# Kernel tuning notes

Hardware: AMD Instinct MI355X
Metric: run time of the kernel (lower is better)

The kernel has to match this reference:

```python
import jax, jax.numpy as jnp
import numpy as np

N_NODES = 50000
N_EDGES = 400000
D_NODE = 256
D_EDGE = 64
LN_EPS = 1e-6  # flax LayerNorm default


def _layer_norm(x, scale, bias):
    mu = jnp.mean(x, axis=-1, keepdims=True)
    var = jnp.mean(jnp.square(x - mu), axis=-1, keepdims=True)
    return (x - mu) * jax.lax.rsqrt(var + LN_EPS) * scale + bias


def _glorot(key, shape):
    fan_in, fan_out = shape
    std = jnp.sqrt(2.0 / (fan_in + fan_out))
    return std * jax.random.normal(key, shape, dtype=jnp.float32)


def setup_inputs() -> dict:
    key = jax.random.key(0)
    ks = jax.random.split(key, 10)
    inp = {
        "nodes": jax.random.normal(ks[0], (N_NODES, D_NODE), dtype=jnp.float32),
        "edges": jax.random.normal(ks[1], (N_EDGES, D_EDGE), dtype=jnp.float32),
        "senders": jax.random.randint(ks[2], (N_EDGES,), 0, N_NODES, dtype=jnp.int32),
        "receivers": jax.random.randint(ks[3], (N_EDGES,), 0, N_NODES, dtype=jnp.int32),
        # message projection (no bias)
        "W_message": _glorot(ks[4], (D_NODE + D_EDGE, D_NODE)),
        # NodeMLP (ReluMLP_skip) with n_features_list_nodes = [256, 256, 256]
        "mlp_W0": _glorot(ks[5], (D_NODE, D_NODE)), "mlp_b0": jnp.zeros((D_NODE,), jnp.float32),
        "mlp_W1": _glorot(ks[6], (D_NODE, D_NODE)), "mlp_b1": jnp.zeros((D_NODE,), jnp.float32),
        "mlp_W2": _glorot(ks[7], (D_NODE, D_NODE)), "mlp_b2": jnp.zeros((D_NODE,), jnp.float32),
        # LayerNorm params
        "ln_aggr_scale": jnp.ones((D_NODE,), jnp.float32), "ln_aggr_bias": jnp.zeros((D_NODE,), jnp.float32),
        "ln_out_scale": jnp.ones((D_NODE,), jnp.float32), "ln_out_bias": jnp.zeros((D_NODE,), jnp.float32),
    }
    return inp


def _relu_mlp_skip(x, Ws, bs):
    # Dense layers; ReLU on all but the last; residual add whenever widths match.
    n = len(Ws)
    for i, (W, b) in enumerate(zip(Ws, bs)):
        y = x @ W + b
        if i < n - 1:
            y = jax.nn.relu(y)
        x = x + y if y.shape[-1] == x.shape[-1] else y
    return x


def reference(nodes, edges, senders, receivers, W_message,
              mlp_W0, mlp_b0, mlp_W1, mlp_b1, mlp_W2, mlp_b2,
              ln_aggr_scale, ln_aggr_bias, ln_out_scale, ln_out_bias):
    total_nodes = nodes.shape[0]
    sender_features = nodes[senders]                      # [E, d] gather
    msg_in = jnp.concatenate([sender_features, edges], axis=-1)  # [E, d+d_e]
    messages = msg_in @ W_message                          # [E, d]
    agg = jax.ops.segment_sum(messages, receivers, num_segments=total_nodes)  # [N, d]
    h = _layer_norm(jax.nn.relu(agg) + nodes, ln_aggr_scale, ln_aggr_bias)
    nodes_out = _relu_mlp_skip(h, [mlp_W0, mlp_W1, mlp_W2], [mlp_b0, mlp_b1, mlp_b2])
    nodes_new = _layer_norm(nodes + nodes_out, ln_out_scale, ln_out_bias)
    return nodes_new
```

## Files before the change

kernel.cpp:

```cpp
#include <hip/hip_runtime.h>

#define NN 50000
#define NE 400000

typedef unsigned short u16;
typedef unsigned int   u32;
typedef __bf16 bf16x4 __attribute__((ext_vector_type(4)));
typedef __bf16 bf16x8 __attribute__((ext_vector_type(8)));
typedef float  f32x4  __attribute__((ext_vector_type(4)));

union ABFrag { bf16x8 v; bf16x4 h[2]; };
union BFrag  { uint4 u; bf16x8 v; };

__device__ __forceinline__ u16 f2bfu(float f) {
  u32 u = __builtin_bit_cast(u32, f);
  return (u16)((u + 0x7FFFu + ((u >> 16) & 1u)) >> 16);
}
__device__ __forceinline__ float bf2f(u16 u) {
  return __builtin_bit_cast(float, (u32)u << 16);
}

__device__ __forceinline__ void pack_one(const float* __restrict__ W,
                                         u16* __restrict__ P, int idx) {
  int k = idx >> 8, n = idx & 255;
  int t = k >> 5, kp = k & 31;
  int g = (kp & 15) >> 2;
  int j = (kp & 3) | ((kp >> 4) << 2);
  P[(((t << 8) + n) << 5) + (g << 3) + j] = f2bfu(W[idx]);
}

#define NB_CVT  12500
#define NB_PACK 1088
#define NB_HIST 1563

__global__ __launch_bounds__(256) void k_prep(
    const float* __restrict__ nodes, u16* __restrict__ nodes_bf,
    const float* __restrict__ Wm, const float* __restrict__ W0,
    const float* __restrict__ W1, const float* __restrict__ W2,
    u16* __restrict__ Pm, u16* __restrict__ P0,
    u16* __restrict__ P1, u16* __restrict__ P2,
    const int* __restrict__ recv, int* __restrict__ cnt)
{
  int b = blockIdx.x, t = threadIdx.x;
  if (b < NB_CVT) {
    int i = b * 256 + t;
    float4 f = ((const float4*)nodes)[i];
    ushort4 o;
    o.x = f2bfu(f.x); o.y = f2bfu(f.y); o.z = f2bfu(f.z); o.w = f2bfu(f.w);
    ((ushort4*)nodes_bf)[i] = o;
  } else if (b < NB_CVT + NB_PACK) {
    int idx = (b - NB_CVT) * 256 + t;
    const int S0 = 320 * 256, S1 = S0 + 65536, S2 = S1 + 65536;
    if (idx < S0)      pack_one(Wm, Pm, idx);
    else if (idx < S1) pack_one(W0, P0, idx - S0);
    else if (idx < S2) pack_one(W1, P1, idx - S1);
    else               pack_one(W2, P2, idx - S2);
  } else {
    int i = (b - NB_CVT - NB_PACK) * 256 + t;
    if (i < NE) atomicAdd(&cnt[recv[i]], 1);
  }
}

__global__ __launch_bounds__(256) void k_scan1(const int* __restrict__ cnt,
                                               int* __restrict__ loc,
                                               int* __restrict__ bsum) {
  __shared__ int sm[256];
  int t = threadIdx.x, i = blockIdx.x * 256 + t;
  int v = (i < NN) ? cnt[i] : 0;
  sm[t] = v;
  __syncthreads();
  #pragma unroll
  for (int d = 1; d < 256; d <<= 1) {
    int x = sm[t];
    int y = (t >= d) ? sm[t - d] : 0;
    __syncthreads();
    sm[t] = x + y;
    __syncthreads();
  }
  if (i < NN) loc[i] = sm[t] - v;
  if (t == 255) bsum[blockIdx.x] = sm[255];
}

__global__ __launch_bounds__(256) void k_scan2(int* __restrict__ bsum,
                                               int* __restrict__ bpre, int nb) {
  __shared__ int sm[256];
  int t = threadIdx.x;
  int v = (t < nb) ? bsum[t] : 0;
  sm[t] = v;
  __syncthreads();
  #pragma unroll
  for (int d = 1; d < 256; d <<= 1) {
    int x = sm[t];
    int y = (t >= d) ? sm[t - d] : 0;
    __syncthreads();
    sm[t] = x + y;
    __syncthreads();
  }
  if (t < nb) bpre[t] = sm[t] - v;
}

__global__ __launch_bounds__(256) void k_scan3(const int* __restrict__ loc,
                                               const int* __restrict__ bpre,
                                               int* __restrict__ offs,
                                               int* __restrict__ cursor) {
  int i = blockIdx.x * 256 + threadIdx.x;
  if (i < NN) {
    int o = loc[i] + bpre[blockIdx.x];
    offs[i] = o;
    cursor[i] = o;
  }
  if (i == NN - 1) offs[NN] = NE;
}

__global__ __launch_bounds__(256) void k_scatter(
    const int* __restrict__ snd, const int* __restrict__ recv,
    int* __restrict__ cursor, int2* __restrict__ s_pair) {
  int e = blockIdx.x * 256 + threadIdx.x;
  if (e < NE) {
    int p = atomicAdd(&cursor[recv[e]], 1);
    int2 pr; pr.x = snd[e]; pr.y = e;
    s_pair[p] = pr;
  }
}

__global__ __launch_bounds__(256) void k_aggr(
    const u16* __restrict__ nodes_bf, const float* __restrict__ edges,
    const int* __restrict__ offs, const int2* __restrict__ s_pair,
    u16* __restrict__ X)
{
  const int node = blockIdx.x * 4 + (threadIdx.x >> 6);
  const int lane = threadIdx.x & 63;
  const int beg = offs[node], end = offs[node + 1];
  float a0 = 0.f, a1 = 0.f, a2 = 0.f, a3 = 0.f, a4 = 0.f;

  for (int jb = beg; jb < end; jb += 8) {
    int j = jb + (lane & 7);
    if (j >= end) j = end - 1;
    int2 pr = s_pair[j];
    const int rem = end - jb;

#define GATHER(K) \
    int s##K = __shfl(pr.x, K); int e##K = __shfl(pr.y, K); \
    ushort4 n##K = *(const ushort4*)(nodes_bf + (size_t)s##K * 256 + (lane << 2)); \
    float v##K = edges[(size_t)e##K * 64 + lane];

    GATHER(0) GATHER(1) GATHER(2) GATHER(3)
    GATHER(4) GATHER(5) GATHER(6) GATHER(7)
#undef GATHER

#define ACCUM(K) \
    if (rem > K) { \
      a0 += bf2f(n##K.x); a1 += bf2f(n##K.y); \
      a2 += bf2f(n##K.z); a3 += bf2f(n##K.w); \
      a4 += v##K; }

    ACCUM(0) ACCUM(1) ACCUM(2) ACCUM(3)
    ACCUM(4) ACCUM(5) ACCUM(6) ACCUM(7)
#undef ACCUM
  }

  u16* xr = X + (size_t)node * 320;
  ushort4 o;
  o.x = f2bfu(a0); o.y = f2bfu(a1); o.z = f2bfu(a2); o.w = f2bfu(a3);
  *(ushort4*)(xr + (lane << 2)) = o;
  xr[256 + lane] = f2bfu(a4);
}

#define AT_ADDR(r, c) (atb + ((((r) * 640) + ((c) * 2)) ^ (((r) & 7) << 4)))

#define WRBT(c, v) do { int _c = (c); \
  int _i = (((_c >> 10) << 13) + ((_c & 3) << 11) + (((_c & 1023) >> 2) << 3)) ^ ((_c & 3) << 4); \
  *(uint4*)&Bt[_i] = (v); } while (0)

#define MFMA_STEP(t) \
  _Pragma("unroll") \
  for (int kk = 0; kk < 2; ++kk) { \
    ABFrag a; \
    const int kc = (((t) * 2 + kk) << 5) + (g << 2); \
    const int m = wr16 + l16; \
    a.h[0] = *(const bf16x4*)AT_ADDR(m, kc); \
    a.h[1] = *(const bf16x4*)AT_ADDR(m, kc + 16); \
    _Pragma("unroll") \
    for (int q = 0; q < 4; ++q) { \
      BFrag b; \
      b.u = *(const uint4*)&Bt[((kk << 13) + (g << 11) + ((wcn + (q << 4) + l16) << 3)) ^ (g << 4)]; \
      acc[q] = __builtin_amdgcn_mfma_f32_16x16x32_bf16(a.v, b.v, acc[q], 0, 0, 0); \
    } \
  }

#define RUN_LAYER(wp, T) do { \
  const u16* pb = (wp) + ((size_t)tid << 3); \
  uint4 p0 = *(const uint4*)(pb); \
  uint4 p1 = *(const uint4*)(pb + 8192); \
  _Pragma("unroll 1") \
  for (int t = 0; t < (T); ++t) { \
    __syncthreads(); \
    WRBT(tid, p0); WRBT(tid + 1024, p1); \
    __syncthreads(); \
    if (t + 1 < (T)) { \
      const u16* nb = pb + ((size_t)(t + 1) << 14); \
      p0 = *(const uint4*)nb; p1 = *(const uint4*)(nb + 8192); \
    } \
    MFMA_STEP(t) \
  } \
} while (0)

#define LN_STATS() do { \
  _Pragma("unroll") \
  for (int r = 0; r < 4; ++r) { \
    float s  = acc[0][r] + acc[1][r] + acc[2][r] + acc[3][r]; \
    float s2 = acc[0][r]*acc[0][r] + acc[1][r]*acc[1][r] + acc[2][r]*acc[2][r] + acc[3][r]*acc[3][r]; \
    s  += __shfl_xor(s, 1);  s  += __shfl_xor(s, 2);  s  += __shfl_xor(s, 4);  s  += __shfl_xor(s, 8); \
    s2 += __shfl_xor(s2, 1); s2 += __shfl_xor(s2, 2); s2 += __shfl_xor(s2, 4); s2 += __shfl_xor(s2, 8); \
    if (l16 == 0) { int m = wr16 + g4 + r; red[m][wc2] = s; red[m][wc2 + 1] = s2; } \
  } \
  __syncthreads(); \
  if (tid < 64) { \
    float s  = red[tid][0] + red[tid][2] + red[tid][4] + red[tid][6]; \
    float s2 = red[tid][1] + red[tid][3] + red[tid][5] + red[tid][7]; \
    float mu  = s * (1.f / 256.f); \
    float var = s2 * (1.f / 256.f) - mu * mu; \
    murs[tid][0] = mu; murs[tid][1] = rsqrtf(var + 1e-6f); \
  } \
  __syncthreads(); \
} while (0)

__global__ __launch_bounds__(1024)
void k_fused(
    const u16* __restrict__ X, const float* __restrict__ nodes,
    const u16* __restrict__ wm, const u16* __restrict__ w0,
    const u16* __restrict__ w1, const u16* __restrict__ w2,
    const float* __restrict__ b0, const float* __restrict__ b1,
    const float* __restrict__ b2,
    const float* __restrict__ lnAs, const float* __restrict__ lnAb,
    const float* __restrict__ lnOs, const float* __restrict__ lnOb,
    float* __restrict__ out)
{
  __shared__ u16 At[64 * 320];
  __shared__ u16 Bt[16384];
  __shared__ float red[64][8];
  __shared__ float murs[64][2];

  const int tid = threadIdx.x;
  const int lane = tid & 63;
  const int w16 = tid >> 6;
  const int wr16 = (w16 >> 2) << 4;
  const int wcn = (w16 & 3) << 6;
  const int wc2 = (w16 & 3) << 1;
  const int l16 = lane & 15, g = lane >> 4, g4 = g << 2;
  const int r0 = blockIdx.x * 64;

  char* const atb = (char*)At;

  #pragma unroll
  for (int it = 0; it < 3; ++it) {
    int c = tid + it * 1024;
    if (c < 2560) {
      int r = c / 40, seg = c - r * 40;
      int row = r0 + r;
      uint4 v = {0u, 0u, 0u, 0u};
      if (row < NN) v = *(const uint4*)(X + (size_t)row * 320 + seg * 8);
      *(uint4*)(atb + ((r * 640 + seg * 16) ^ ((r & 7) << 4))) = v;
    }
  }

  f32x4 acc[4];
  const f32x4 z = {0.f, 0.f, 0.f, 0.f};
  #pragma unroll
  for (int q = 0; q < 4; ++q) acc[q] = z;

  RUN_LAYER(wm, 5);

  #pragma unroll
  for (int q = 0; q < 4; ++q) {
    int n = wcn + (q << 4) + l16;
    #pragma unroll
    for (int r = 0; r < 4; ++r) {
      int row = r0 + wr16 + g4 + r;
      float nv = (row < NN) ? nodes[(size_t)row * 256 + n] : 0.f;
      acc[q][r] = fmaxf(acc[q][r], 0.f) + nv;
    }
  }
  LN_STATS();
  #pragma unroll
  for (int q = 0; q < 4; ++q) {
    int n = wcn + (q << 4) + l16;
    float scl = lnAs[n], bia = lnAb[n];
    #pragma unroll
    for (int r = 0; r < 4; ++r) {
      int m = wr16 + g4 + r;
      float h = (acc[q][r] - murs[m][0]) * murs[m][1] * scl + bia;
      *(u16*)AT_ADDR(m, n) = f2bfu(h);
      acc[q][r] = 0.f;
    }
  }

  #pragma unroll 1
  for (int l = 0; l < 3; ++l) {
    const u16* wp = (l == 0) ? w0 : (l == 1) ? w1 : w2;
    RUN_LAYER(wp, 4);
    __syncthreads();

    if (l < 2) {
      const float* bp = (l == 0) ? b0 : b1;
      #pragma unroll
      for (int q = 0; q < 4; ++q) {
        int n = wcn + (q << 4) + l16;
        float bn = bp[n];
        #pragma unroll
        for (int r = 0; r < 4; ++r) {
          int m = wr16 + g4 + r;
          u16* p = (u16*)AT_ADDR(m, n);
          float xn = bf2f(*p) + fmaxf(acc[q][r] + bn, 0.f);
          *p = f2bfu(xn);
          acc[q][r] = 0.f;
        }
      }
    } else {
      #pragma unroll
      for (int q = 0; q < 4; ++q) {
        int n = wcn + (q << 4) + l16;
        float bn = b2[n];
        #pragma unroll
        for (int r = 0; r < 4; ++r) {
          int m = wr16 + g4 + r;
          int row = r0 + m;
          float nv = (row < NN) ? nodes[(size_t)row * 256 + n] : 0.f;
          acc[q][r] = nv + bf2f(*(const u16*)AT_ADDR(m, n)) + acc[q][r] + bn;
        }
      }
    }
  }

  LN_STATS();
  #pragma unroll
  for (int q = 0; q < 4; ++q) {
    int n = wcn + (q << 4) + l16;
    float scl = lnOs[n], bia = lnOb[n];
    #pragma unroll
    for (int r = 0; r < 4; ++r) {
      int m = wr16 + g4 + r;
      int row = r0 + m;
      if (row < NN)
        out[(size_t)row * 256 + n] =
            (acc[q][r] - murs[m][0]) * murs[m][1] * scl + bia;
    }
  }
}

extern "C" void kernel_launch(void* const* d_in, const int* in_sizes, int n_in,
                              void* d_out, int out_size, void* d_ws, size_t ws_size,
                              hipStream_t stream)
{
  const float* nodes = (const float*)d_in[0];
  const float* edges = (const float*)d_in[1];
  const int* senders = (const int*)d_in[2];
  const int* receivers = (const int*)d_in[3];
  const float* Wmsg = (const float*)d_in[4];
  const float* W0 = (const float*)d_in[5];
  const float* b0 = (const float*)d_in[6];
  const float* W1 = (const float*)d_in[7];
  const float* b1 = (const float*)d_in[8];
  const float* W2 = (const float*)d_in[9];
  const float* b2 = (const float*)d_in[10];
  const float* lnAs = (const float*)d_in[11];
  const float* lnAb = (const float*)d_in[12];
  const float* lnOs = (const float*)d_in[13];
  const float* lnOb = (const float*)d_in[14];
  float* out = (float*)d_out;
  (void)in_sizes; (void)n_in; (void)out_size; (void)ws_size;

  char* w = (char*)d_ws;
  size_t off = 0;
  auto take = [&](size_t b) { void* p = w + off; off += (b + 511) & ~(size_t)511; return p; };

  u16*   nodes_bf = (u16*)take((size_t)NN * 256 * 2);
  u16*   wmsg_p   = (u16*)take(320 * 256 * 2);
  u16*   w0_p     = (u16*)take(256 * 256 * 2);
  u16*   w1_p     = (u16*)take(256 * 256 * 2);
  u16*   w2_p     = (u16*)take(256 * 256 * 2);
  u16*   X        = (u16*)take((size_t)NN * 320 * 2);
  int*   cnt      = (int*)take((size_t)NN * 4);
  int*   loc      = (int*)take((size_t)NN * 4);
  int*   offs     = (int*)take((size_t)(NN + 1) * 4);
  int*   cursor   = (int*)take((size_t)NN * 4);
  int2*  s_pair   = (int2*)take((size_t)NE * 8);
  int*   bsum     = (int*)take(256 * 4);
  int*   bpre     = (int*)take(256 * 4);

  const int NB = (NN + 255) / 256;

  hipMemsetAsync(cnt, 0, (size_t)NN * 4, stream);
  k_prep<<<NB_CVT + NB_PACK + NB_HIST, 256, 0, stream>>>(
      nodes, nodes_bf, Wmsg, W0, W1, W2, wmsg_p, w0_p, w1_p, w2_p,
      receivers, cnt);

  k_scan1<<<NB, 256, 0, stream>>>(cnt, loc, bsum);
  k_scan2<<<1, 256, 0, stream>>>(bsum, bpre, NB);
  k_scan3<<<NB, 256, 0, stream>>>(loc, bpre, offs, cursor);
  k_scatter<<<(NE + 255) / 256, 256, 0, stream>>>(senders, receivers, cursor, s_pair);

  k_aggr<<<NN / 4, 256, 0, stream>>>(nodes_bf, edges, offs, s_pair, X);

  const int MB = (NN + 63) / 64;
  k_fused<<<MB, 1024, 0, stream>>>(X, nodes, wmsg_p, w0_p, w1_p, w2_p,
                                   b0, b1, b2, lnAs, lnAb, lnOs, lnOb, out);
}
```

Measured before the change: 225.7 us.

## Read MFMA weight fragments from global directly and split aggregation across four waves

```diff
diff --git a/kernel.cpp b/kernel.cpp
--- a/kernel.cpp
+++ b/kernel.cpp
@@ -128,80 +128,52 @@
     const int* __restrict__ offs, const int2* __restrict__ s_pair,
     u16* __restrict__ X)
 {
-  const int node = blockIdx.x * 4 + (threadIdx.x >> 6);
-  const int lane = threadIdx.x & 63;
+  __shared__ float part[4][5][64];
+  const int node = blockIdx.x;
+  const int w = threadIdx.x >> 6, lane = threadIdx.x & 63;
   const int beg = offs[node], end = offs[node + 1];
+
   float a0 = 0.f, a1 = 0.f, a2 = 0.f, a3 = 0.f, a4 = 0.f;
-
-  for (int jb = beg; jb < end; jb += 8) {
-    int j = jb + (lane & 7);
-    if (j >= end) j = end - 1;
+  for (int j = beg + w; j < end; j += 4) {
     int2 pr = s_pair[j];
-    const int rem = end - jb;
-
-#define GATHER(K) \
-    int s##K = __shfl(pr.x, K); int e##K = __shfl(pr.y, K); \
-    ushort4 n##K = *(const ushort4*)(nodes_bf + (size_t)s##K * 256 + (lane << 2)); \
-    float v##K = edges[(size_t)e##K * 64 + lane];
-
-    GATHER(0) GATHER(1) GATHER(2) GATHER(3)
-    GATHER(4) GATHER(5) GATHER(6) GATHER(7)
-#undef GATHER
-
-#define ACCUM(K) \
-    if (rem > K) { \
-      a0 += bf2f(n##K.x); a1 += bf2f(n##K.y); \
-      a2 += bf2f(n##K.z); a3 += bf2f(n##K.w); \
-      a4 += v##K; }
-
-    ACCUM(0) ACCUM(1) ACCUM(2) ACCUM(3)
-    ACCUM(4) ACCUM(5) ACCUM(6) ACCUM(7)
-#undef ACCUM
-  }
-
-  u16* xr = X + (size_t)node * 320;
-  ushort4 o;
-  o.x = f2bfu(a0); o.y = f2bfu(a1); o.z = f2bfu(a2); o.w = f2bfu(a3);
-  *(ushort4*)(xr + (lane << 2)) = o;
-  xr[256 + lane] = f2bfu(a4);
+    ushort4 nv = *(const ushort4*)(nodes_bf + (size_t)pr.x * 256 + (lane << 2));
+    float ev = edges[(size_t)pr.y * 64 + lane];
+    a0 += bf2f(nv.x); a1 += bf2f(nv.y); a2 += bf2f(nv.z); a3 += bf2f(nv.w);
+    a4 += ev;
+  }
+  part[w][0][lane] = a0; part[w][1][lane] = a1; part[w][2][lane] = a2;
+  part[w][3][lane] = a3; part[w][4][lane] = a4;
+  __syncthreads();
+  if (w == 0) {
+    a0 = part[0][0][lane] + part[1][0][lane] + part[2][0][lane] + part[3][0][lane];
+    a1 = part[0][1][lane] + part[1][1][lane] + part[2][1][lane] + part[3][1][lane];
+    a2 = part[0][2][lane] + part[1][2][lane] + part[2][2][lane] + part[3][2][lane];
+    a3 = part[0][3][lane] + part[1][3][lane] + part[2][3][lane] + part[3][3][lane];
+    a4 = part[0][4][lane] + part[1][4][lane] + part[2][4][lane] + part[3][4][lane];
+    u16* xr = X + (size_t)node * 320;
+    ushort4 o;
+    o.x = f2bfu(a0); o.y = f2bfu(a1); o.z = f2bfu(a2); o.w = f2bfu(a3);
+    *(ushort4*)(xr + (lane << 2)) = o;
+    xr[256 + lane] = f2bfu(a4);
+  }
 }
 
 #define AT_ADDR(r, c) (atb + ((((r) * 640) + ((c) * 2)) ^ (((r) & 7) << 4)))
 
-#define WRBT(c, v) do { int _c = (c); \
-  int _i = (((_c >> 10) << 13) + ((_c & 3) << 11) + (((_c & 1023) >> 2) << 3)) ^ ((_c & 3) << 4); \
-  *(uint4*)&Bt[_i] = (v); } while (0)
-
-#define MFMA_STEP(t) \
-  _Pragma("unroll") \
-  for (int kk = 0; kk < 2; ++kk) { \
+#define RUN_LAYER_G(wp, T) do { \
+  _Pragma("unroll 1") \
+  for (int t = 0; t < (T); ++t) { \
     ABFrag a; \
-    const int kc = (((t) * 2 + kk) << 5) + (g << 2); \
+    const int kc = ((t) << 5) + (g << 2); \
     const int m = wr16 + l16; \
     a.h[0] = *(const bf16x4*)AT_ADDR(m, kc); \
     a.h[1] = *(const bf16x4*)AT_ADDR(m, kc + 16); \
     _Pragma("unroll") \
     for (int q = 0; q < 4; ++q) { \
       BFrag b; \
-      b.u = *(const uint4*)&Bt[((kk << 13) + (g << 11) + ((wcn + (q << 4) + l16) << 3)) ^ (g << 4)]; \
+      b.u = *(const uint4*)((wp) + ((size_t)((((t) << 8) + wcn + (q << 4) + l16) << 5)) + (g << 3)); \
       acc[q] = __builtin_amdgcn_mfma_f32_16x16x32_bf16(a.v, b.v, acc[q], 0, 0, 0); \
     } \
-  }
-
-#define RUN_LAYER(wp, T) do { \
-  const u16* pb = (wp) + ((size_t)tid << 3); \
-  uint4 p0 = *(const uint4*)(pb); \
-  uint4 p1 = *(const uint4*)(pb + 8192); \
-  _Pragma("unroll 1") \
-  for (int t = 0; t < (T); ++t) { \
-    __syncthreads(); \
-    WRBT(tid, p0); WRBT(tid + 1024, p1); \
-    __syncthreads(); \
-    if (t + 1 < (T)) { \
-      const u16* nb = pb + ((size_t)(t + 1) << 14); \
-      p0 = *(const uint4*)nb; p1 = *(const uint4*)(nb + 8192); \
-    } \
-    MFMA_STEP(t) \
   } \
 } while (0)
 
@@ -237,7 +209,6 @@
     float* __restrict__ out)
 {
   __shared__ u16 At[64 * 320];
-  __shared__ u16 Bt[16384];
   __shared__ float red[64][8];
   __shared__ float murs[64][2];
 
@@ -269,7 +240,9 @@
   #pragma unroll
   for (int q = 0; q < 4; ++q) acc[q] = z;
 
-  RUN_LAYER(wm, 5);
+  __syncthreads();
+
+  RUN_LAYER_G(wm, 10);
 
   #pragma unroll
   for (int q = 0; q < 4; ++q) {
@@ -294,11 +267,12 @@
       acc[q][r] = 0.f;
     }
   }
+  __syncthreads();
 
   #pragma unroll 1
   for (int l = 0; l < 3; ++l) {
     const u16* wp = (l == 0) ? w0 : (l == 1) ? w1 : w2;
-    RUN_LAYER(wp, 4);
+    RUN_LAYER_G(wp, 8);
     __syncthreads();
 
     if (l < 2) {
@@ -316,6 +290,7 @@
           acc[q][r] = 0.f;
         }
       }
+      __syncthreads();
     } else {
       #pragma unroll
       for (int q = 0; q < 4; ++q) {
@@ -400,7 +375,7 @@
   k_scan3<<<NB, 256, 0, stream>>>(loc, bpre, offs, cursor);
   k_scatter<<<(NE + 255) / 256, 256, 0, stream>>>(senders, receivers, cursor, s_pair);
 
-  k_aggr<<<NN / 4, 256, 0, stream>>>(nodes_bf, edges, offs, s_pair, X);
+  k_aggr<<<NN, 256, 0, stream>>>(nodes_bf, edges, offs, s_pair, X);
 
   const int MB = (NN + 63) / 64;
   k_fused<<<MB, 1024, 0, stream>>>(X, nodes, wmsg_p, w0_p, w1_p, w2_p,
```

Result: slower. 321.3 us (+42.4%).
